# Kernel tuning notes

Measured on AMD Instinct MI355X. Metric: run time of the kernel, lower is better.

Reference implementation:

```python
import jax, jax.numpy as jnp
import numpy as np

NUM_HEADS = 12
HEAD_DIM = 64
HIDDEN = 768
QMAX = 127.0  # 8-bit symmetric
DOMAIN_MIN, DOMAIN_MAX = -10.0, 0.0
NUM_INTERVALS = 12


def _build_pla_coeffs():
    xs = np.linspace(DOMAIN_MIN, DOMAIN_MAX, 1001)
    ys = np.exp(xs)
    intervals = np.linspace(DOMAIN_MIN, DOMAIN_MAX, NUM_INTERVALS + 1)
    ms, cs = [], []
    for i in range(NUM_INTERVALS):
        a, b = intervals[i], intervals[i + 1]
        mask = (xs >= a) & (xs <= b)
        m, c = np.polyfit(xs[mask], ys[mask], 1)
        ms.append(m)
        cs.append(c)
    return (jnp.asarray(ms, jnp.float32), jnp.asarray(cs, jnp.float32),
            jnp.asarray(intervals, jnp.float32))

COEFFS_M, COEFFS_C, INTERVALS = _build_pla_coeffs()


def quantize(x):
    # per-row (last-dim) abs-max symmetric 8-bit fake quant
    max_val = jnp.max(jnp.abs(x), axis=-1, keepdims=True)
    scale = max_val / QMAX
    scale = jnp.where(scale == 0, 1.0, scale)
    return jnp.clip(jnp.round(x / scale), -QMAX, QMAX) * scale


def to_fixed_point(x, bits=32, frac_bits=26):
    scale = 2.0 ** frac_bits
    lo = -2.0 ** (bits - 1)
    hi = 2.0 ** (bits - 1) - 1
    return jnp.clip(jnp.round(x * scale), lo, hi) / scale


def pla_exp(x):
    xc = jnp.clip(x, DOMAIN_MIN, DOMAIN_MAX)
    # sum(x >= intervals) - 1 == searchsorted(intervals, x, 'right') - 1
    idx = jnp.clip(jnp.searchsorted(INTERVALS, xc, side='right') - 1, 0, NUM_INTERVALS - 1)
    return COEFFS_M[idx] * xc + COEFFS_C[idx]


def pla_softmax(scores):
    shifted = scores - jnp.max(scores, axis=-1, keepdims=True)
    shifted_fx = to_fixed_point(shifted, 32, 26)
    exps = pla_exp(shifted_fx)
    sm = exps / (jnp.sum(exps, axis=-1, keepdims=True) + 1e-9)
    return quantize(sm)


def q_linear(x, W, b):
    # QuantizedLinear: quantize input and weight (per-row), fp bias
    return quantize(x) @ quantize(W).T + b


def split_heads(x):
    B, S, _ = x.shape
    return x.reshape(B, S, NUM_HEADS, HEAD_DIM).transpose(0, 2, 1, 3)  # bhsd


def mhsa(hidden_states, Wq, bq, Wk, bk, Wv, bv, Wo, bo):
    B, S, H = hidden_states.shape
    scale = HEAD_DIM ** -0.5
    q = split_heads(q_linear(hidden_states, Wq, bq))
    k = split_heads(q_linear(hidden_states, Wk, bk))
    v = split_heads(q_linear(hidden_states, Wv, bv))
    # per-row quantization makes tile-wise quant identical to full quant
    scores = jnp.einsum('bhqd,bhkd->bhqk', quantize(q), quantize(k)) * scale
    probs = pla_softmax(scores)
    ctx = jnp.einsum('bhqk,bhkd->bhqd', probs, quantize(v))
    ctx = ctx.transpose(0, 2, 1, 3).reshape(B, S, H)
    return q_linear(ctx, Wo, bo)


def setup_inputs() -> dict:
    key = jax.random.key(0)
    ks = jax.random.split(key, 9)
    B, S = 8, 512
    hs = jax.random.normal(ks[0], (B, S, HIDDEN), dtype=jnp.float32)
    def w(k):
        return jax.random.normal(k, (HIDDEN, HIDDEN), dtype=jnp.float32) * 0.02
    def b(k):
        return jax.random.normal(k, (HIDDEN,), dtype=jnp.float32) * 0.02
    return {
        'hidden_states': hs,
        'Wq': w(ks[1]), 'bq': b(ks[2]),
        'Wk': w(ks[3]), 'bk': b(ks[4]),
        'Wv': w(ks[5]), 'bv': b(ks[6]),
        'Wo': w(ks[7]), 'bo': b(ks[8]),
    }


def reference(hidden_states, Wq, bq, Wk, bk, Wv, bv, Wo, bo):
    return mhsa(hidden_states, Wq, bq, Wk, bk, Wv, bv, Wo, bo)
```

## Files before the change

### kernel.cpp

```cpp
#include <hip/hip_runtime.h>
#include <cmath>

#define R_TOT 4096
#define HID   768
#define NHEAD 12
#define HDIM  64
#define SEQ   512
#define BATCH 8

typedef int   v4i  __attribute__((ext_vector_type(4)));
typedef float v4f  __attribute__((ext_vector_type(4)));
typedef _Float16 half8 __attribute__((ext_vector_type(8)));
typedef _Float16 half4v __attribute__((ext_vector_type(4)));

struct PlaConsts { float m[12]; float c[12]; float b[13]; };

static PlaConsts build_pla() {
  PlaConsts pc;
  const int NPTS = 1001;
  static double xs[NPTS], ys[NPTS];
  const double step = 10.0 / 1000.0;
  for (int j = 0; j < NPTS; ++j) xs[j] = (double)j * step + (-10.0);
  xs[NPTS - 1] = 0.0;
  for (int j = 0; j < NPTS; ++j) ys[j] = std::exp(xs[j]);
  double bnd[13];
  const double step2 = 10.0 / 12.0;
  for (int k = 0; k < 13; ++k) bnd[k] = (double)k * step2 + (-10.0);
  bnd[12] = 0.0;
  for (int i = 0; i < 12; ++i) {
    const double a = bnd[i], bb = bnd[i + 1];
    double sx = 0, sy = 0; int n = 0;
    for (int j = 0; j < NPTS; ++j)
      if (xs[j] >= a && xs[j] <= bb) { sx += xs[j]; sy += ys[j]; ++n; }
    const double xm = sx / n, ym = sy / n;
    double sxx = 0, sxy = 0;
    for (int j = 0; j < NPTS; ++j)
      if (xs[j] >= a && xs[j] <= bb) {
        const double dx = xs[j] - xm;
        sxx += dx * dx; sxy += dx * (ys[j] - ym);
      }
    const double m = sxy / sxx;
    pc.m[i] = (float)m;
    pc.c[i] = (float)(ym - m * xm);
  }
  for (int k = 0; k < 13; ++k) pc.b[k] = (float)bnd[k];
  return pc;
}
static const PlaConsts g_pla = build_pla();

__device__ __forceinline__ void quant_row_body(const float* __restrict__ x,
                                               signed char* __restrict__ qrow,
                                               float* __restrict__ srow,
                                               int ncols) {
  float m = 0.f;
  for (int c = threadIdx.x; c < ncols; c += 256)
    m = fmaxf(m, fabsf(x[c]));
  #pragma unroll
  for (int off = 32; off; off >>= 1) m = fmaxf(m, __shfl_xor(m, off));
  __shared__ float red[4];
  const int lane = threadIdx.x & 63, wv = threadIdx.x >> 6;
  if (lane == 0) red[wv] = m;
  __syncthreads();
  if (threadIdx.x == 0) {
    float mm = fmaxf(fmaxf(red[0], red[1]), fmaxf(red[2], red[3]));
    float s = mm / 127.0f;
    if (s == 0.f) s = 1.f;
    red[0] = s;
    *srow = s;
  }
  __syncthreads();
  const float s = red[0];
  for (int c = threadIdx.x; c < ncols; c += 256) {
    float q = rintf(x[c] / s);
    q = fminf(fmaxf(q, -127.f), 127.f);
    qrow[c] = (signed char)(int)q;
  }
}

__global__ __launch_bounds__(256)
void quant_rows(const float* __restrict__ src, int ncols,
                signed char* __restrict__ qout, float* __restrict__ sout) {
  const int row = blockIdx.x;
  quant_row_body(src + (size_t)row * ncols, qout + (size_t)row * ncols,
                 sout + row, ncols);
}

__global__ __launch_bounds__(256)
void quant_all(const float* hs, const float* w0, const float* w1,
               const float* w2, const float* w3,
               signed char* qx, float* sx,
               signed char* q0, signed char* q1, signed char* q2, signed char* q3,
               float* s0, float* s1, float* s2, float* s3) {
  const int bid = blockIdx.x;
  const float* src; signed char* qo; float* so; int row;
  if (bid < R_TOT)            { src = hs; qo = qx; so = sx; row = bid; }
  else if (bid < R_TOT + 768) { src = w0; qo = q0; so = s0; row = bid - R_TOT; }
  else if (bid < R_TOT + 1536){ src = w1; qo = q1; so = s1; row = bid - R_TOT - 768; }
  else if (bid < R_TOT + 2304){ src = w2; qo = q2; so = s2; row = bid - R_TOT - 1536; }
  else                        { src = w3; qo = q3; so = s3; row = bid - R_TOT - 2304; }
  quant_row_body(src + (size_t)row * HID, qo + (size_t)row * HID, so + row, HID);
}

__device__ __forceinline__
void proj_body(int mode,
               const signed char* __restrict__ qx, const float* __restrict__ sx,
               const signed char* __restrict__ qw, const float* __restrict__ sw,
               const float* __restrict__ bias,
               signed char* __restrict__ qo, float* __restrict__ so,
               _Float16* __restrict__ vt, float* __restrict__ fo,
               signed char* Al, signed char* Bl) {
  const int tid = threadIdx.x;
  const int w = tid >> 6, lane = tid & 63;
  const int n = lane & 15, quad = lane >> 4;
  const int row0 = blockIdx.x * 128, col0 = blockIdx.y * 64;
  const int ar = tid >> 1, ac = (tid & 1) * 64;
  const int br = tid >> 2, bc = (tid & 3) * 32;
  v4i acc[2][4];
  #pragma unroll
  for (int s = 0; s < 2; ++s)
    #pragma unroll
    for (int j = 0; j < 4; ++j) acc[s][j] = (v4i){0, 0, 0, 0};
  for (int k0 = 0; k0 < HID; k0 += 128) {
    const signed char* ap = qx + (size_t)(row0 + ar) * HID + k0 + ac;
    const int4 a0 = *(const int4*)(ap);
    const int4 a1 = *(const int4*)(ap + 16);
    const int4 a2 = *(const int4*)(ap + 32);
    const int4 a3 = *(const int4*)(ap + 48);
    const signed char* bp = qw + (size_t)(col0 + br) * HID + k0 + bc;
    const int4 b0 = *(const int4*)(bp);
    const int4 b1 = *(const int4*)(bp + 16);
    if (k0) __syncthreads();
    *(int4*)&Al[ar * 144 + ac]      = a0;
    *(int4*)&Al[ar * 144 + ac + 16] = a1;
    *(int4*)&Al[ar * 144 + ac + 32] = a2;
    *(int4*)&Al[ar * 144 + ac + 48] = a3;
    *(int4*)&Bl[br * 144 + bc]      = b0;
    *(int4*)&Bl[br * 144 + bc + 16] = b1;
    __syncthreads();
    #pragma unroll
    for (int ks = 0; ks < 128; ks += 64) {
      const v4i af0 = *(const v4i*)&Al[(w * 16 + n) * 144 + ks + quad * 16];
      const v4i af1 = *(const v4i*)&Al[(64 + w * 16 + n) * 144 + ks + quad * 16];
      #pragma unroll
      for (int j = 0; j < 4; ++j) {
        const v4i bf = *(const v4i*)&Bl[(j * 16 + n) * 144 + ks + quad * 16];
        acc[0][j] = __builtin_amdgcn_mfma_i32_16x16x64_i8(af0, bf, acc[0][j], 0, 0, 0);
        acc[1][j] = __builtin_amdgcn_mfma_i32_16x16x64_i8(af1, bf, acc[1][j], 0, 0, 0);
      }
    }
  }
  float swc4[4], bc4[4];
  #pragma unroll
  for (int j = 0; j < 4; ++j) {
    swc4[j] = sw[col0 + j * 16 + n];
    bc4[j] = bias[col0 + j * 16 + n];
  }
  #pragma unroll
  for (int s = 0; s < 2; ++s) {
    const int mrow = s * 64 + w * 16 + quad * 4;
    float sxr[4];
    #pragma unroll
    for (int r = 0; r < 4; ++r) sxr[r] = sx[row0 + mrow + r];
    float vals[4][4];
    #pragma unroll
    for (int j = 0; j < 4; ++j)
      #pragma unroll
      for (int r = 0; r < 4; ++r)
        vals[j][r] = (float)acc[s][j][r] * (sxr[r] * swc4[j]) + bc4[j];
    if (mode == 1) {
      const int h = blockIdx.y;
      #pragma unroll
      for (int r = 0; r < 4; ++r) {
        float m = 0.f;
        #pragma unroll
        for (int j = 0; j < 4; ++j) m = fmaxf(m, fabsf(vals[j][r]));
        #pragma unroll
        for (int off = 1; off < 16; off <<= 1) m = fmaxf(m, __shfl_xor(m, off));
        float sq = m / 127.0f;
        if (sq == 0.f) sq = 1.f;
        const int grow = row0 + mrow + r;
        const int bidx = grow >> 9, sidx = grow & 511;
        const size_t rowidx = ((size_t)bidx * NHEAD + h) * SEQ + sidx;
        #pragma unroll
        for (int j = 0; j < 4; ++j) {
          float q = fminf(fmaxf(rintf(vals[j][r] / sq), -127.f), 127.f);
          qo[rowidx * HDIM + j * 16 + n] = (signed char)(int)q;
        }
        if (n == 0) so[rowidx] = sq;
      }
    } else if (mode == 2) {
      const int h = blockIdx.y;
      float srow[4];
      #pragma unroll
      for (int r = 0; r < 4; ++r) {
        float m = 0.f;
        #pragma unroll
        for (int j = 0; j < 4; ++j) m = fmaxf(m, fabsf(vals[j][r]));
        #pragma unroll
        for (int off = 1; off < 16; off <<= 1) m = fmaxf(m, __shfl_xor(m, off));
        float sq = m / 127.0f;
        if (sq == 0.f) sq = 1.f;
        srow[r] = sq;
      }
      const int grow0 = row0 + mrow;
      const int bidx = grow0 >> 9, sidx = grow0 & 511;
      const int kb = sidx >> 5, ko = sidx & 31;
      const size_t hbv = (size_t)bidx * NHEAD + h;
      #pragma unroll
      for (int j = 0; j < 4; ++j) {
        half4v hv;
        #pragma unroll
        for (int r = 0; r < 4; ++r) {
          float q = fminf(fmaxf(rintf(vals[j][r] / srow[r]), -127.f), 127.f);
          hv[r] = (_Float16)(q * srow[r]);
        }
        *(half4v*)(vt + ((hbv * 16 + kb) * 64 + j * 16 + n) * 32 + ko) = hv;
      }
    } else {
      #pragma unroll
      for (int r = 0; r < 4; ++r) {
        const size_t base = (size_t)(row0 + mrow + r) * HID + col0;
        #pragma unroll
        for (int j = 0; j < 4; ++j)
          fo[base + j * 16 + n] = vals[j][r];
      }
    }
  }
}

__global__ __launch_bounds__(256)
void proj_qkv(const signed char* __restrict__ qx, const float* __restrict__ sx,
              const signed char* qwq, const float* swq, const float* bq,
              signed char* qqd, float* qqs,
              const signed char* qwk, const float* swk, const float* bk,
              signed char* qkd, float* qks,
              const signed char* qwv, const float* swv, const float* bv,
              _Float16* vt2) {
  __shared__ __align__(16) signed char Al[128 * 144];
  __shared__ __align__(16) signed char Bl[64 * 144];
  if (blockIdx.z == 0)
    proj_body(1, qx, sx, qwq, swq, bq, qqd, qqs, nullptr, nullptr, Al, Bl);
  else if (blockIdx.z == 1)
    proj_body(1, qx, sx, qwk, swk, bk, qkd, qks, nullptr, nullptr, Al, Bl);
  else
    proj_body(2, qx, sx, qwv, swv, bv, nullptr, nullptr, vt2, nullptr, Al, Bl);
}

__global__ __launch_bounds__(256)
void proj_out(const signed char* __restrict__ qx, const float* __restrict__ sx,
              const signed char* qw, const float* sw, const float* bias,
              float* fo) {
  __shared__ __align__(16) signed char Al[128 * 144];
  __shared__ __align__(16) signed char Bl[64 * 144];
  proj_body(0, qx, sx, qw, sw, bias, nullptr, nullptr, nullptr, fo, Al, Bl);
}

#define PSTR 520
__global__ __launch_bounds__(256)
void attn_kernel(const signed char* __restrict__ qq, const float* __restrict__ qss,
                 const signed char* __restrict__ qk, const float* __restrict__ kss,
                 const _Float16* __restrict__ vt2,
                 float* __restrict__ ctx, const PlaConsts pc) {
  __shared__ __align__(16) _Float16 PhT[16 * PSTR];
  __shared__ __align__(16) float red_max[2][16][4];
  __shared__ __align__(16) float red_sum[2][16][4];
  __shared__ __align__(16) float red_amax[2][16][4];
  __shared__ float psa[2][16];
  __shared__ __align__(8) float pb2[12][2];
  __shared__ __align__(8) float pmc[12][2];

  const int tid = threadIdx.x;
  const int q0 = blockIdx.x * 32;
  const int hh = blockIdx.y, bz = blockIdx.z;
  const size_t hb = (size_t)bz * NHEAD + hh;
  const signed char* qqh = qq + (hb * SEQ + q0) * HDIM;
  const signed char* qkh = qk + hb * SEQ * HDIM;
  const float* ksp = kss + hb * SEQ;

  if (tid < 12) {
    pb2[tid][0] = pc.b[tid]; pb2[tid][1] = pc.b[tid + 1];
    pmc[tid][0] = pc.m[tid]; pmc[tid][1] = pc.c[tid];
  }

  const int w = tid >> 6, lane = tid & 63;
  const int n = lane & 15, quad = lane >> 4;

  float s26[2][8][4];
  {
    const v4i qf0 = *(const v4i*)(qqh + (size_t)n * HDIM + quad * 16);
    const v4i qf1 = *(const v4i*)(qqh + (size_t)(16 + n) * HDIM + quad * 16);
    const float qs0 = (qss[hb * SEQ + q0 + n] * 0.125f) * 67108864.0f;
    const float qs1 = (qss[hb * SEQ + q0 + 16 + n] * 0.125f) * 67108864.0f;
    float vmax0 = -3.0e38f, vmax1 = -3.0e38f;
    #pragma unroll
    for (int t = 0; t < 8; ++t) {
      const int kc0 = (t * 4 + w) * 16;
      const v4i kfrag = *(const v4i*)(qkh + (size_t)(kc0 + n) * HDIM + quad * 16);
      const float4 ks4 = *(const float4*)(ksp + kc0 + quad * 4);
      v4i zero = {};
      const v4i a0 = __builtin_amdgcn_mfma_i32_16x16x64_i8(kfrag, qf0, zero, 0, 0, 0);
      const v4i a1 = __builtin_amdgcn_mfma_i32_16x16x64_i8(kfrag, qf1, zero, 0, 0, 0);
      const float ks[4] = {ks4.x, ks4.y, ks4.z, ks4.w};
      #pragma unroll
      for (int r = 0; r < 4; ++r) {
        const float v0 = (float)a0[r] * (qs0 * ks[r]);
        const float v1 = (float)a1[r] * (qs1 * ks[r]);
        s26[0][t][r] = v0; vmax0 = fmaxf(vmax0, v0);
        s26[1][t][r] = v1; vmax1 = fmaxf(vmax1, v1);
      }
    }
    vmax0 = fmaxf(vmax0, __shfl_xor(vmax0, 16));
    vmax0 = fmaxf(vmax0, __shfl_xor(vmax0, 32));
    vmax1 = fmaxf(vmax1, __shfl_xor(vmax1, 16));
    vmax1 = fmaxf(vmax1, __shfl_xor(vmax1, 32));
    if (quad == 0) { red_max[0][n][w] = vmax0; red_max[1][n][w] = vmax1; }
  }
  __syncthreads();

  #pragma unroll
  for (int tau = 0; tau < 2; ++tau) {
    const float4 rm = *(const float4*)&red_max[tau][n][0];
    const float mx26 = fmaxf(fmaxf(rm.x, rm.y), fmaxf(rm.z, rm.w));
    float sum = 0.f, amax = 0.f;
    #pragma unroll
    for (int t = 0; t < 8; ++t) {
      #pragma unroll
      for (int r = 0; r < 4; ++r) {
        float sh = s26[tau][t][r] - mx26;
        sh = fmaxf(sh, -671088640.0f);
        const float tq = rintf(sh);
        const float xc = tq * 1.4901161193847656e-08f;
        int g = (int)floorf((xc + 10.0f) * 1.2f);
        g = g < 0 ? 0 : (g > 11 ? 11 : g);
        const float2 bb = *(const float2*)&pb2[g][0];
        if (xc < bb.x) --g;
        else if (xc >= bb.y) ++g;
        g = g < 0 ? 0 : (g > 11 ? 11 : g);
        const float2 mc = *(const float2*)&pmc[g][0];
        const float e = __fadd_rn(__fmul_rn(mc.x, xc), mc.y);
        s26[tau][t][r] = e;
        sum += e;
        amax = fmaxf(amax, fabsf(e));
      }
    }
    sum += __shfl_xor(sum, 16);
    sum += __shfl_xor(sum, 32);
    amax = fmaxf(amax, __shfl_xor(amax, 16));
    amax = fmaxf(amax, __shfl_xor(amax, 32));
    if (quad == 0) { red_sum[tau][n][w] = sum; red_amax[tau][n][w] = amax; }
  }
  __syncthreads();

  #pragma unroll
  for (int tau = 0; tau < 2; ++tau) {
    {
      const float4 rs = *(const float4*)&red_sum[tau][n][0];
      const float4 ra = *(const float4*)&red_amax[tau][n][0];
      float denom = (rs.x + rs.y) + (rs.z + rs.w);
      denom = __fadd_rn(denom, 1e-9f);
      const float rden = 1.0f / denom;
      const float am = fmaxf(fmaxf(ra.x, ra.y), fmaxf(ra.z, ra.w));
      float ps = (am * rden) / 127.0f;
      if (ps == 0.f) ps = 1.f;
      const float rps = 1.0f / ps;
      if (w == 0 && quad == 0) psa[tau][n] = ps;
      #pragma unroll
      for (int t = 0; t < 8; ++t) {
        half4v hq;
        #pragma unroll
        for (int r = 0; r < 4; ++r) {
          const float p = s26[tau][t][r] * rden;
          const float qf = fminf(fmaxf(rintf(p * rps), -127.f), 127.f);
          hq[r] = (_Float16)qf;
        }
        *(half4v*)&PhT[n * PSTR + (t * 4 + w) * 16 + quad * 4] = hq;
      }
    }
    __syncthreads();
    {
      v4f acc0 = {0.f, 0.f, 0.f, 0.f};
      const _Float16* vbase = vt2 + ((size_t)hb * 16 * 64 + (w * 16 + n)) * 32 + quad * 8;
      const _Float16* p0 = &PhT[n * PSTR + quad * 8];
      #pragma unroll 4
      for (int kt = 0; kt < 16; ++kt) {
        const half8 bf = *(const half8*)(vbase + kt * 2048);
        acc0 = __builtin_amdgcn_mfma_f32_16x16x32_f16(*(const half8*)(p0 + kt * 32), bf, acc0, 0, 0, 0);
      }
      #pragma unroll
      for (int r = 0; r < 4; ++r) {
        const int row = quad * 4 + r;
        ctx[((size_t)bz * SEQ + q0 + tau * 16 + row) * HID + (size_t)hh * HDIM + w * 16 + n] =
            acc0[r] * psa[tau][row];
      }
    }
    if (tau == 0) __syncthreads();
  }
}

extern "C" void kernel_launch(void* const* d_in, const int* in_sizes, int n_in,
                              void* d_out, int out_size, void* d_ws, size_t ws_size,
                              hipStream_t stream) {
  (void)in_sizes; (void)n_in; (void)out_size; (void)ws_size;
  const float* hs = (const float*)d_in[0];
  const float* Wq = (const float*)d_in[1];
  const float* bq = (const float*)d_in[2];
  const float* Wk = (const float*)d_in[3];
  const float* bk = (const float*)d_in[4];
  const float* Wv = (const float*)d_in[5];
  const float* bv = (const float*)d_in[6];
  const float* Wo = (const float*)d_in[7];
  const float* bo = (const float*)d_in[8];
  float* out = (float*)d_out;

  char* ws = (char*)d_ws;
  size_t off = 0;
  auto alloc = [&](size_t bytes) -> char* {
    char* p = ws + off;
    off += (bytes + 255) & ~(size_t)255;
    return p;
  };
  signed char* qx  = (signed char*)alloc((size_t)R_TOT * HID);
  float*       sx  = (float*)alloc((size_t)R_TOT * 4);
  signed char* qwq = (signed char*)alloc((size_t)HID * HID);
  signed char* qwk = (signed char*)alloc((size_t)HID * HID);
  signed char* qwv = (signed char*)alloc((size_t)HID * HID);
  signed char* qwo = (signed char*)alloc((size_t)HID * HID);
  float*       swq = (float*)alloc((size_t)HID * 4);
  float*       swk = (float*)alloc((size_t)HID * 4);
  float*       swv = (float*)alloc((size_t)HID * 4);
  float*       swo = (float*)alloc((size_t)HID * 4);
  signed char* qqd = (signed char*)alloc((size_t)R_TOT * HID);
  float*       qqs = (float*)alloc((size_t)BATCH * NHEAD * SEQ * 4);
  signed char* qkd = (signed char*)alloc((size_t)R_TOT * HID);
  float*       qks = (float*)alloc((size_t)BATCH * NHEAD * SEQ * 4);
  float*       ctx = (float*)alloc((size_t)R_TOT * HID * 4);
  _Float16*    vt2 = (_Float16*)alloc((size_t)BATCH * NHEAD * HDIM * SEQ * 2);
  signed char* qc  = qx;
  float*       scs = sx;

  quant_all<<<R_TOT + 4 * HID, 256, 0, stream>>>(
      hs, Wq, Wk, Wv, Wo, qx, sx,
      qwq, qwk, qwv, qwo, swq, swk, swv, swo);

  proj_qkv<<<dim3(R_TOT / 128, HID / 64, 3), 256, 0, stream>>>(
      qx, sx, qwq, swq, bq, qqd, qqs,
      qwk, swk, bk, qkd, qks,
      qwv, swv, bv, vt2);

  attn_kernel<<<dim3(SEQ / 32, NHEAD, BATCH), 256, 0, stream>>>(
      qqd, qqs, qkd, qks, vt2, ctx, g_pla);

  quant_rows<<<R_TOT, 256, 0, stream>>>(ctx, HID, qc, scs);
  proj_out<<<dim3(R_TOT / 128, HID / 64), 256, 0, stream>>>(
      qc, scs, qwo, swo, bo, out);
}
```

Measured before the change: 162.7 us.

## Interleave softmax and PV tiles in attention, simplify row quant and PLA lookup

The attention kernel now double-buffers the probability tile in shared memory so that the exp of the second 16-row tile and the quantization of its probabilities are interleaved with the PV MFMA of the first tile, with one fewer barrier overall. The PLA segment lookup packs bounds and coefficients into one float4 table and reloads only when the neighbour check changes the segment. Probability quantization folds the normalization into a single 127/amax multiplier. This reassociation can change rounding of some quantized probabilities relative to the reference. The row quantizer is specialized to 768 columns, keeping values in registers instead of reading the row twice.

```diff
diff --git a/kernel.cpp b/kernel.cpp
--- a/kernel.cpp
+++ b/kernel.cpp
@@ -50,11 +50,11 @@
 
 __device__ __forceinline__ void quant_row_body(const float* __restrict__ x,
                                                signed char* __restrict__ qrow,
-                                               float* __restrict__ srow,
-                                               int ncols) {
-  float m = 0.f;
-  for (int c = threadIdx.x; c < ncols; c += 256)
-    m = fmaxf(m, fabsf(x[c]));
+                                               float* __restrict__ srow) {
+  const float v0 = x[threadIdx.x];
+  const float v1 = x[threadIdx.x + 256];
+  const float v2 = x[threadIdx.x + 512];
+  float m = fmaxf(fmaxf(fabsf(v0), fabsf(v1)), fabsf(v2));
   #pragma unroll
   for (int off = 32; off; off >>= 1) m = fmaxf(m, __shfl_xor(m, off));
   __shared__ float red[4];
@@ -70,19 +70,19 @@
   }
   __syncthreads();
   const float s = red[0];
-  for (int c = threadIdx.x; c < ncols; c += 256) {
-    float q = rintf(x[c] / s);
-    q = fminf(fmaxf(q, -127.f), 127.f);
-    qrow[c] = (signed char)(int)q;
-  }
+  qrow[threadIdx.x] =
+      (signed char)(int)fminf(fmaxf(rintf(v0 / s), -127.f), 127.f);
+  qrow[threadIdx.x + 256] =
+      (signed char)(int)fminf(fmaxf(rintf(v1 / s), -127.f), 127.f);
+  qrow[threadIdx.x + 512] =
+      (signed char)(int)fminf(fmaxf(rintf(v2 / s), -127.f), 127.f);
 }
 
 __global__ __launch_bounds__(256)
-void quant_rows(const float* __restrict__ src, int ncols,
+void quant_rows(const float* __restrict__ src,
                 signed char* __restrict__ qout, float* __restrict__ sout) {
   const int row = blockIdx.x;
-  quant_row_body(src + (size_t)row * ncols, qout + (size_t)row * ncols,
-                 sout + row, ncols);
+  quant_row_body(src + (size_t)row * HID, qout + (size_t)row * HID, sout + row);
 }
 
 __global__ __launch_bounds__(256)
@@ -98,7 +98,7 @@
   else if (bid < R_TOT + 1536){ src = w1; qo = q1; so = s1; row = bid - R_TOT - 768; }
   else if (bid < R_TOT + 2304){ src = w2; qo = q2; so = s2; row = bid - R_TOT - 1536; }
   else                        { src = w3; qo = q3; so = s3; row = bid - R_TOT - 2304; }
-  quant_row_body(src + (size_t)row * HID, qo + (size_t)row * HID, so + row, HID);
+  quant_row_body(src + (size_t)row * HID, qo + (size_t)row * HID, so + row);
 }
 
 __device__ __forceinline__
@@ -255,19 +255,75 @@
   proj_body(0, qx, sx, qw, sw, bias, nullptr, nullptr, nullptr, fo, Al, Bl);
 }
 
+__device__ __forceinline__
+void softmax_exp_tile(float (&s)[8][4], float mx26, const float4* __restrict__ pt4,
+                      float& sum_out, float& amax_out) {
+  float sum = 0.f, amax = 0.f;
+  #pragma unroll
+  for (int t = 0; t < 8; ++t) {
+    #pragma unroll
+    for (int r = 0; r < 4; ++r) {
+      float sh = s[t][r] - mx26;
+      sh = fmaxf(sh, -671088640.0f);
+      const float tq = rintf(sh);
+      const float xc = tq * 1.4901161193847656e-08f;
+      int g = (int)((xc + 10.0f) * 1.2f);
+      g = g > 11 ? 11 : g;
+      float4 E = pt4[g];
+      int gn = g + ((xc >= E.y) ? 1 : 0) - ((xc < E.x) ? 1 : 0);
+      gn = gn < 0 ? 0 : (gn > 11 ? 11 : gn);
+      if (gn != g) E = pt4[gn];
+      const float e = __fadd_rn(__fmul_rn(E.z, xc), E.w);
+      s[t][r] = e;
+      sum += e;
+      amax = fmaxf(amax, fabsf(e));
+    }
+  }
+  sum += __shfl_xor(sum, 16);
+  sum += __shfl_xor(sum, 32);
+  amax = fmaxf(amax, __shfl_xor(amax, 16));
+  amax = fmaxf(amax, __shfl_xor(amax, 32));
+  sum_out = sum; amax_out = amax;
+}
+
+__device__ __forceinline__
+void quant_pack_tile(const float (&s)[8][4], float t127,
+                     _Float16* __restrict__ phtrow, int w, int quad) {
+  #pragma unroll
+  for (int t = 0; t < 8; ++t) {
+    half4v hq;
+    #pragma unroll
+    for (int r = 0; r < 4; ++r) {
+      const float qf = fminf(fmaxf(rintf(s[t][r] * t127), -127.f), 127.f);
+      hq[r] = (_Float16)qf;
+    }
+    *(half4v*)&phtrow[(t * 4 + w) * 16 + quad * 4] = hq;
+  }
+}
+
+__device__ __forceinline__
+v4f pv_tile(const _Float16* __restrict__ vbase, const _Float16* __restrict__ prow) {
+  v4f acc = {0.f, 0.f, 0.f, 0.f};
+  #pragma unroll
+  for (int kt = 0; kt < 16; ++kt) {
+    const half8 bf = *(const half8*)(vbase + kt * 2048);
+    acc = __builtin_amdgcn_mfma_f32_16x16x32_f16(*(const half8*)(prow + kt * 32), bf, acc, 0, 0, 0);
+  }
+  return acc;
+}
+
 #define PSTR 520
 __global__ __launch_bounds__(256)
 void attn_kernel(const signed char* __restrict__ qq, const float* __restrict__ qss,
                  const signed char* __restrict__ qk, const float* __restrict__ kss,
                  const _Float16* __restrict__ vt2,
                  float* __restrict__ ctx, const PlaConsts pc) {
-  __shared__ __align__(16) _Float16 PhT[16 * PSTR];
+  __shared__ __align__(16) _Float16 PhT[2][16 * PSTR];
   __shared__ __align__(16) float red_max[2][16][4];
   __shared__ __align__(16) float red_sum[2][16][4];
   __shared__ __align__(16) float red_amax[2][16][4];
   __shared__ float psa[2][16];
-  __shared__ __align__(8) float pb2[12][2];
-  __shared__ __align__(8) float pmc[12][2];
+  __shared__ __align__(16) float4 pt4[12];
 
   const int tid = threadIdx.x;
   const int q0 = blockIdx.x * 32;
@@ -277,10 +333,8 @@
   const signed char* qkh = qk + hb * SEQ * HDIM;
   const float* ksp = kss + hb * SEQ;
 
-  if (tid < 12) {
-    pb2[tid][0] = pc.b[tid]; pb2[tid][1] = pc.b[tid + 1];
-    pmc[tid][0] = pc.m[tid]; pmc[tid][1] = pc.c[tid];
-  }
+  if (tid < 12)
+    pt4[tid] = make_float4(pc.b[tid], pc.b[tid + 1], pc.m[tid], pc.c[tid]);
 
   const int w = tid >> 6, lane = tid & 63;
   const int n = lane & 15, quad = lane >> 4;
@@ -317,83 +371,70 @@
   }
   __syncthreads();
 
-  #pragma unroll
-  for (int tau = 0; tau < 2; ++tau) {
-    const float4 rm = *(const float4*)&red_max[tau][n][0];
+  {
+    const float4 rm = *(const float4*)&red_max[0][n][0];
     const float mx26 = fmaxf(fmaxf(rm.x, rm.y), fmaxf(rm.z, rm.w));
-    float sum = 0.f, amax = 0.f;
-    #pragma unroll
-    for (int t = 0; t < 8; ++t) {
-      #pragma unroll
-      for (int r = 0; r < 4; ++r) {
-        float sh = s26[tau][t][r] - mx26;
-        sh = fmaxf(sh, -671088640.0f);
-        const float tq = rintf(sh);
-        const float xc = tq * 1.4901161193847656e-08f;
-        int g = (int)floorf((xc + 10.0f) * 1.2f);
-        g = g < 0 ? 0 : (g > 11 ? 11 : g);
-        const float2 bb = *(const float2*)&pb2[g][0];
-        if (xc < bb.x) --g;
-        else if (xc >= bb.y) ++g;
-        g = g < 0 ? 0 : (g > 11 ? 11 : g);
-        const float2 mc = *(const float2*)&pmc[g][0];
-        const float e = __fadd_rn(__fmul_rn(mc.x, xc), mc.y);
-        s26[tau][t][r] = e;
-        sum += e;
-        amax = fmaxf(amax, fabsf(e));
-      }
-    }
-    sum += __shfl_xor(sum, 16);
-    sum += __shfl_xor(sum, 32);
-    amax = fmaxf(amax, __shfl_xor(amax, 16));
-    amax = fmaxf(amax, __shfl_xor(amax, 32));
-    if (quad == 0) { red_sum[tau][n][w] = sum; red_amax[tau][n][w] = amax; }
-  }
-  __syncthreads();
-
-  #pragma unroll
-  for (int tau = 0; tau < 2; ++tau) {
-    {
-      const float4 rs = *(const float4*)&red_sum[tau][n][0];
-      const float4 ra = *(const float4*)&red_amax[tau][n][0];
-      float denom = (rs.x + rs.y) + (rs.z + rs.w);
-      denom = __fadd_rn(denom, 1e-9f);
-      const float rden = 1.0f / denom;
-      const float am = fmaxf(fmaxf(ra.x, ra.y), fmaxf(ra.z, ra.w));
-      float ps = (am * rden) / 127.0f;
-      if (ps == 0.f) ps = 1.f;
-      const float rps = 1.0f / ps;
-      if (w == 0 && quad == 0) psa[tau][n] = ps;
-      #pragma unroll
-      for (int t = 0; t < 8; ++t) {
-        half4v hq;
-        #pragma unroll
-        for (int r = 0; r < 4; ++r) {
-          const float p = s26[tau][t][r] * rden;
-          const float qf = fminf(fmaxf(rintf(p * rps), -127.f), 127.f);
-          hq[r] = (_Float16)qf;
-        }
-        *(half4v*)&PhT[n * PSTR + (t * 4 + w) * 16 + quad * 4] = hq;
-      }
-    }
-    __syncthreads();
-    {
-      v4f acc0 = {0.f, 0.f, 0.f, 0.f};
-      const _Float16* vbase = vt2 + ((size_t)hb * 16 * 64 + (w * 16 + n)) * 32 + quad * 8;
-      const _Float16* p0 = &PhT[n * PSTR + quad * 8];
-      #pragma unroll 4
-      for (int kt = 0; kt < 16; ++kt) {
-        const half8 bf = *(const half8*)(vbase + kt * 2048);
-        acc0 = __builtin_amdgcn_mfma_f32_16x16x32_f16(*(const half8*)(p0 + kt * 32), bf, acc0, 0, 0, 0);
-      }
-      #pragma unroll
-      for (int r = 0; r < 4; ++r) {
-        const int row = quad * 4 + r;
-        ctx[((size_t)bz * SEQ + q0 + tau * 16 + row) * HID + (size_t)hh * HDIM + w * 16 + n] =
-            acc0[r] * psa[tau][row];
-      }
-    }
-    if (tau == 0) __syncthreads();
+    float sum, amax;
+    softmax_exp_tile(s26[0], mx26, pt4, sum, amax);
+    if (quad == 0) { red_sum[0][n][w] = sum; red_amax[0][n][w] = amax; }
+  }
+  __syncthreads();
+
+  {
+    const float4 rs = *(const float4*)&red_sum[0][n][0];
+    const float4 ra = *(const float4*)&red_amax[0][n][0];
+    float denom = (rs.x + rs.y) + (rs.z + rs.w);
+    denom = __fadd_rn(denom, 1e-9f);
+    const float rden = 1.0f / denom;
+    const float am = fmaxf(fmaxf(ra.x, ra.y), fmaxf(ra.z, ra.w));
+    float ps = (am * rden) / 127.0f;
+    if (ps == 0.f) ps = 1.f;
+    if (w == 0 && quad == 0) psa[0][n] = ps;
+    const float t127 = 127.0f / am;
+    quant_pack_tile(s26[0], t127, &PhT[0][n * PSTR], w, quad);
+
+    const float4 rm = *(const float4*)&red_max[1][n][0];
+    const float mx26 = fmaxf(fmaxf(rm.x, rm.y), fmaxf(rm.z, rm.w));
+    float sum, amax;
+    softmax_exp_tile(s26[1], mx26, pt4, sum, amax);
+    if (quad == 0) { red_sum[1][n][w] = sum; red_amax[1][n][w] = amax; }
+  }
+  __syncthreads();
+
+  const _Float16* vbase = vt2 + ((size_t)hb * 16 * 64 + (w * 16 + n)) * 32 + quad * 8;
+
+  {
+    const v4f acc0 = pv_tile(vbase, &PhT[0][n * PSTR + quad * 8]);
+
+    const float4 rs = *(const float4*)&red_sum[1][n][0];
+    const float4 ra = *(const float4*)&red_amax[1][n][0];
+    float denom = (rs.x + rs.y) + (rs.z + rs.w);
+    denom = __fadd_rn(denom, 1e-9f);
+    const float rden = 1.0f / denom;
+    const float am = fmaxf(fmaxf(ra.x, ra.y), fmaxf(ra.z, ra.w));
+    float ps = (am * rden) / 127.0f;
+    if (ps == 0.f) ps = 1.f;
+    if (w == 0 && quad == 0) psa[1][n] = ps;
+    const float t127 = 127.0f / am;
+    quant_pack_tile(s26[1], t127, &PhT[1][n * PSTR], w, quad);
+
+    #pragma unroll
+    for (int r = 0; r < 4; ++r) {
+      const int row = quad * 4 + r;
+      ctx[((size_t)bz * SEQ + q0 + row) * HID + (size_t)hh * HDIM + w * 16 + n] =
+          acc0[r] * psa[0][row];
+    }
+  }
+  __syncthreads();
+
+  {
+    const v4f acc1 = pv_tile(vbase, &PhT[1][n * PSTR + quad * 8]);
+    #pragma unroll
+    for (int r = 0; r < 4; ++r) {
+      const int row = quad * 4 + r;
+      ctx[((size_t)bz * SEQ + q0 + 16 + row) * HID + (size_t)hh * HDIM + w * 16 + n] =
+          acc1[r] * psa[1][row];
+    }
   }
 }
 
@@ -450,7 +491,7 @@
   attn_kernel<<<dim3(SEQ / 32, NHEAD, BATCH), 256, 0, stream>>>(
       qqd, qqs, qkd, qks, vt2, ctx, g_pla);
 
-  quant_rows<<<R_TOT, 256, 0, stream>>>(ctx, HID, qc, scs);
+  quant_rows<<<R_TOT, 256, 0, stream>>>(ctx, qc, scs);
   proj_out<<<dim3(R_TOT / 128, HID / 64), 256, 0, stream>>>(
       qc, scs, qwo, swo, bo, out);
 }
```

Measured after the change: 153.7 us. 5.6% less time.
